# Optimization experiments

Measured on AMD Instinct MI355X. Metric: run time of the kernel, lower is better.

## Reference

```python
import jax, jax.numpy as jnp
import numpy as np
from jax import lax

N, T, D, W, H, V = 256, 64, 1280, 256, 512, 10000
NULL_IDX = 0  # ignore_index


def setup_inputs() -> dict:
    key = jax.random.key(0)
    ks = jax.random.split(key, 9)
    features = jax.random.normal(ks[0], (N, D), dtype=jnp.float32)
    captions = jax.random.randint(ks[1], (N, T + 1), 0, V, dtype=jnp.int64)
    # learned parameters
    W_proj = jax.random.normal(ks[2], (D, H), dtype=jnp.float32) / np.sqrt(D)
    b_proj = jnp.zeros((H,), dtype=jnp.float32)
    W_embed = jax.random.normal(ks[3], (V, W), dtype=jnp.float32) / np.sqrt(V)
    Wx = jax.random.normal(ks[4], (W, H), dtype=jnp.float32) / np.sqrt(W)
    Wh = jax.random.normal(ks[5], (H, H), dtype=jnp.float32) / np.sqrt(H)
    b = jnp.zeros((H,), dtype=jnp.float32)
    W_out = jax.random.normal(ks[6], (H, V), dtype=jnp.float32) / np.sqrt(H)
    b_out = jnp.zeros((V,), dtype=jnp.float32)
    return {"features": features, "captions": captions, "W_proj": W_proj,
            "b_proj": b_proj, "W_embed": W_embed, "Wx": Wx, "Wh": Wh, "b": b,
            "W_out": W_out, "b_out": b_out}


def reference(features, captions, W_proj, b_proj, W_embed, Wx, Wh, b, W_out, b_out):
    captions_in = captions[:, :-1]   # (N, T)
    captions_out = captions[:, 1:]   # (N, T)

    h0 = features @ W_proj + b_proj                      # (N, H)
    x = W_embed[captions_in]                             # (N, T, W)
    # Precompute input-to-hidden part; recurrence only needs h @ Wh.
    xWxb = jnp.einsum('ntw,wh->nth', x, Wx) + b          # (N, T, H)

    def step(h_prev, xt):
        h_next = jnp.tanh(h_prev @ Wh + xt)
        return h_next, h_next

    _, hs = lax.scan(step, h0, jnp.swapaxes(xWxb, 0, 1))  # (T, N, H)
    h = jnp.swapaxes(hs, 0, 1)                            # (N, T, H)

    scores = jnp.einsum('nth,hv->ntv', h, W_out) + b_out  # (N, T, V)
    logp = jax.nn.log_softmax(scores, axis=-1)
    nll = -jnp.take_along_axis(logp, captions_out[..., None], axis=-1)[..., 0]
    mask = (captions_out != NULL_IDX).astype(nll.dtype)
    loss = jnp.sum(nll * mask) / N
    return loss
```

## Files before the change

kernel.cpp:

```cpp
#include <hip/hip_runtime.h>
#include <hip/hip_bf16.h>
#include <hip/hip_fp8.h>

#define NB 256
#define TT 64
#define DD 1280
#define WW 256
#define HH 512
#define VV 10000
#define VP 10112
#define NCT 79
#define MROWS (NB*TT)

typedef short short8 __attribute__((ext_vector_type(8)));
typedef float f32x4 __attribute__((ext_vector_type(4)));
typedef int   int4v __attribute__((ext_vector_type(4)));
typedef int   int8v __attribute__((ext_vector_type(8)));

static __device__ __forceinline__ unsigned short f2bf(float x){
    unsigned int u = __float_as_uint(x);
    unsigned int r = u + 0x7FFFu + ((u >> 16) & 1u);
    return (unsigned short)(r >> 16);
}
static __device__ __forceinline__ float bf2f(unsigned short u){
    return __uint_as_float(((unsigned int)u) << 16);
}
static __device__ __forceinline__ unsigned char f2f8(float x){
    __hip_fp8_e4m3 q(x);
    return (unsigned char)q.__x;
}
static __device__ __forceinline__ unsigned enc4(float x){
    unsigned s = (x < 0.f) ? 8u : 0u;
    float a = fabsf(x);
    unsigned m;
    if      (a < 0.25f) m = 0;
    else if (a < 0.75f) m = 1;
    else if (a < 1.25f) m = 2;
    else if (a < 1.75f) m = 3;
    else if (a < 2.5f)  m = 4;
    else if (a < 3.5f)  m = 5;
    else if (a < 5.0f)  m = 6;
    else                m = 7;
    return s | m;
}
static __device__ __forceinline__ void gload16b(const unsigned char* g, unsigned char* l){
    __builtin_amdgcn_global_load_lds(
        (const __attribute__((address_space(1))) void*)g,
        (__attribute__((address_space(3))) void*)l, 16, 0, 0);
}


__global__ __launch_bounds__(256) void k_convbf(const float* __restrict__ in,
                                                unsigned short* __restrict__ out, int n4){
    int i = blockIdx.x*256 + threadIdx.x;
    if (i < n4){
        float4 f = *reinterpret_cast<const float4*>(in + (size_t)i*4);
        unsigned short* o = out + (size_t)i*4;
        o[0]=f2bf(f.x); o[1]=f2bf(f.y); o[2]=f2bf(f.z); o[3]=f2bf(f.w);
    }
}

__global__ __launch_bounds__(256) void k_transpose_bf(const float* __restrict__ in,
                                                      unsigned short* __restrict__ out,
                                                      int R, int C, int Cp){
    __shared__ unsigned short tile[64][17];
    int r0 = blockIdx.y*16, c0 = blockIdx.x*64;
    int tid = threadIdx.x;
    int c = tid & 63, rr = tid >> 6;
    #pragma unroll
    for (int j = 0; j < 4; ++j){
        int r = rr + j*4;
        unsigned short v = 0;
        if (r0 + r < R && c0 + c < C) v = f2bf(in[(size_t)(r0+r)*C + c0 + c]);
        tile[c][r] = v;
    }
    __syncthreads();
    int rw = tid & 15, cw = tid >> 4;
    #pragma unroll
    for (int j = 0; j < 4; ++j){
        int c2 = cw + j*16;
        if (c0 + c2 < Cp && r0 + rw < R)
            out[(size_t)(c0+c2)*R + r0 + rw] = tile[c2][rw];
    }
}

__global__ __launch_bounds__(256) void k_transpose_f8(const float* __restrict__ in,
                                                      unsigned char* __restrict__ out,
                                                      int R, int C, int Cp){
    __shared__ unsigned char tile[64][20];
    int r0 = blockIdx.y*16, c0 = blockIdx.x*64;
    int tid = threadIdx.x;
    int c = tid & 63, rr = tid >> 6;
    #pragma unroll
    for (int j = 0; j < 4; ++j){
        int r = rr + j*4;
        unsigned char v = 0;
        if (r0 + r < R && c0 + c < C) v = f2f8(in[(size_t)(r0+r)*C + c0 + c]);
        tile[c][r] = v;
    }
    __syncthreads();
    int rw = tid & 15, cw = tid >> 4;
    #pragma unroll
    for (int j = 0; j < 4; ++j){
        int c2 = cw + j*16;
        int col = c0 + c2, k = r0 + rw;
        if (col < Cp && k < R){
            size_t addr = ((size_t)((col >> 7)*4 + (k >> 7)))*16384
                        + (unsigned)((col & 127)*128 + (k & 127));
            out[addr] = tile[c2][rw];
        }
    }
}

__global__ __launch_bounds__(512) void k_wh4(const float* __restrict__ Wh,
                                             unsigned char* __restrict__ WhT4){
    int j = blockIdx.x;
    int col = threadIdx.x;
    float w0 = Wh[(size_t)(2*j  )*HH + col] * 32.0f;
    float w1 = Wh[(size_t)(2*j+1)*HH + col] * 32.0f;
    WhT4[(size_t)col*256 + j] = (unsigned char)(enc4(w0) | (enc4(w1) << 4));
}

__global__ __launch_bounds__(256) void k_biaspad(const float* __restrict__ bo, float* __restrict__ bop){
    int i = blockIdx.x*256 + threadIdx.x;
    if (i < VP) bop[i] = (i < VV) ? bo[i] : -30000.0f;
}

__global__ __launch_bounds__(512) void k_h0(const float* __restrict__ feat,
                                            const unsigned short* __restrict__ Wpb,
                                            const float* __restrict__ bp,
                                            float* __restrict__ h0){
    int n0 = blockIdx.x*2;
    int h = threadIdx.x;
    const float* f0 = feat + (size_t)(n0+0)*DD;
    const float* f1 = feat + (size_t)(n0+1)*DD;
    float a0=0.f, a1=0.f;
    for (int d = 0; d < DD; d += 4){
        #pragma unroll
        for (int j = 0; j < 4; ++j){
            float w = bf2f(Wpb[(size_t)(d+j)*HH + h]);
            a0 += f0[d+j]*w;
            a1 += f1[d+j]*w;
        }
    }
    float bb = bp[h];
    h0[(size_t)(n0+0)*HH+h] = a0+bb;
    h0[(size_t)(n0+1)*HH+h] = a1+bb;
}

__global__ __launch_bounds__(256) void k_e2(const float* __restrict__ We,
                                            const unsigned short* __restrict__ WxT,
                                            const float* __restrict__ bias,
                                            unsigned short* __restrict__ E2b){
    int lane = threadIdx.x & 63;
    int wv   = threadIdx.x >> 6;
    int l15 = lane & 15, lhi = lane >> 4;
    int rbase = blockIdx.x*64 + wv*16;
    int arow = rbase + l15; if (arow > VV-1) arow = VV-1;
    short8 a[8];
    #pragma unroll
    for (int kk = 0; kk < 8; ++kk){
        const float* src = We + (size_t)arow*WW + kk*32 + lhi*8;
        float4 g0 = *reinterpret_cast<const float4*>(src);
        float4 g1 = *reinterpret_cast<const float4*>(src + 4);
        short8 v;
        v[0]=(short)f2bf(g0.x); v[1]=(short)f2bf(g0.y); v[2]=(short)f2bf(g0.z); v[3]=(short)f2bf(g0.w);
        v[4]=(short)f2bf(g1.x); v[5]=(short)f2bf(g1.y); v[6]=(short)f2bf(g1.z); v[7]=(short)f2bf(g1.w);
        a[kk] = v;
    }
    int ct0 = blockIdx.y*16;
    for (int ct = ct0; ct < ct0+16; ++ct){
        int c0 = ct*16;
        f32x4 acc = {0.f,0.f,0.f,0.f};
        #pragma unroll
        for (int kk = 0; kk < 8; ++kk){
            short8 b = *reinterpret_cast<const short8*>(WxT + (size_t)(c0 + l15)*WW + kk*32 + lhi*8);
            acc = __builtin_amdgcn_mfma_f32_16x16x32_bf16(a[kk], b, acc, 0, 0, 0);
        }
        float bb = bias[c0 + l15];
        #pragma unroll
        for (int r = 0; r < 4; ++r){
            int row = rbase + lhi*4 + r;
            if (row < VV) E2b[(size_t)row*HH + c0 + l15] = f2bf(acc[r] + bb);
        }
    }
}

__global__ __launch_bounds__(512, 2) void k_rnn(const float* __restrict__ h0,
                                                const unsigned char* __restrict__ WhT4,
                                                const unsigned short* __restrict__ E2b,
                                                const int* __restrict__ caps,
                                                unsigned char* __restrict__ hA8){
    __shared__ __align__(32) unsigned char hl[2][HH];
    int tid = threadIdx.x;
    int lane = tid & 63, wv = tid >> 6;
    int l15 = lane & 15, lhi = lane >> 4;
    int n = blockIdx.x;
    int c0w = wv*64;
    int mycol = c0w + lane;
    unsigned char* hbase = hA8 + ((size_t)((n>>1)*4 + (wv>>1)))*16384
                               + (unsigned)((n&1)*64*128 + (mycol & 127));

    int4v b[4][4];
    #pragma unroll
    for (int ct = 0; ct < 4; ++ct){
        int col = c0w + ct*16 + l15;
        #pragma unroll
        for (int kt = 0; kt < 4; ++kt){
            b[ct][kt] = *reinterpret_cast<const int4v*>(WhT4 + (size_t)col*256 + kt*64 + lhi*16);
            asm volatile("" : "+v"(b[ct][kt]));
        }
    }
    hl[0][tid] = f2f8(h0[(size_t)n*HH + tid]);
    __syncthreads();
    int cur = 0;
    for (int t = 0; t < TT; ++t){
        int tok = caps[n*(TT+1) + t];
        unsigned short xv = E2b[(size_t)tok*HH + mycol];
        int8v a[4];
        #pragma unroll
        for (int kt = 0; kt < 4; ++kt)
            a[kt] = *reinterpret_cast<const int8v*>(&hl[cur][kt*128 + lhi*32]);
        f32x4 acc[4];
        #pragma unroll
        for (int ct = 0; ct < 4; ++ct){
            acc[ct] = (f32x4){0.f,0.f,0.f,0.f};
            #pragma unroll
            for (int kt = 0; kt < 4; ++kt){
                int8v bb = __builtin_shufflevector(b[ct][kt], b[ct][kt], 0,1,2,3,0,1,2,3);
                acc[ct] = __builtin_amdgcn_mfma_scale_f32_16x16x128_f8f6f4(
                    a[kt], bb, acc[ct],
                    0, 4,
                    0, (int)0x7F7F7F7F,
                    0, (int)0x7A7A7A7A);
            }
        }
        float v = (lhi == 0) ? acc[0][0] : (lhi == 1) ? acc[1][0]
                : (lhi == 2) ? acc[2][0] : acc[3][0];
        float x = v + bf2f(xv);
        float e = __expf(2.f*x);
        float th = 1.f - 2.f/(e + 1.f);
        unsigned char hv = f2f8(th);
        hl[cur^1][mycol] = hv;
        hbase[t*128] = hv;
        __syncthreads();
        cur ^= 1;
    }
}

__global__ __launch_bounds__(256) void k_scores(const unsigned char* __restrict__ hA8,
                                                const unsigned char* __restrict__ WoT8p,
                                                const float* __restrict__ bop,
                                                const int* __restrict__ caps,
                                                float* __restrict__ pps,
                                                float* __restrict__ pts){
    __shared__ unsigned char As[128*128];
    __shared__ unsigned char Bs[128*128];
    int bid = blockIdx.x;
    int x = bid & 7;
    int local = bid >> 3;
    int ct = local >> 4;
    int rt = x*16 + (local & 15);

    int tid = threadIdx.x;
    int lane = tid & 63, wv = tid >> 6;
    int l15 = lane & 15, lhi = lane >> 4;
    int wr = wv >> 1, wc = wv & 1;
    const unsigned char* Abase = hA8   + (size_t)rt*65536;
    const unsigned char* Bbase = WoT8p + (size_t)ct*65536;

    unsigned coff[4];
    #pragma unroll
    for (int i = 0; i < 4; ++i){
        unsigned chunk = (unsigned)(i*256 + tid);
        unsigned rowloc = chunk >> 3;
        coff[i] = rowloc*128 + (((chunk & 7u) ^ (rowloc & 7u))*16u);
    }

    f32x4 acc[4][4];
    #pragma unroll
    for (int m = 0; m < 4; ++m)
        #pragma unroll
        for (int n = 0; n < 4; ++n)
            acc[m][n] = (f32x4){0.f,0.f,0.f,0.f};

    for (int kt = 0; kt < 4; ++kt){
        #pragma unroll
        for (int i = 0; i < 4; ++i){
            gload16b(Abase + kt*16384 + coff[i], As + (unsigned)((i*256 + wv*64) * 16));
            gload16b(Bbase + kt*16384 + coff[i], Bs + (unsigned)((i*256 + wv*64) * 16));
        }
        __syncthreads();
        int8v af[4], bf[4];
        #pragma unroll
        for (int m = 0; m < 4; ++m){
            unsigned row = (unsigned)(wr*64 + m*16 + l15);
            int4v c0 = *reinterpret_cast<const int4v*>(As + row*128 + (((unsigned)(lhi*2+0) ^ (row&7))*16));
            int4v c1 = *reinterpret_cast<const int4v*>(As + row*128 + (((unsigned)(lhi*2+1) ^ (row&7))*16));
            af[m] = __builtin_shufflevector(c0, c1, 0,1,2,3,4,5,6,7);
        }
        #pragma unroll
        for (int n = 0; n < 4; ++n){
            unsigned col = (unsigned)(wc*64 + n*16 + l15);
            int4v c0 = *reinterpret_cast<const int4v*>(Bs + col*128 + (((unsigned)(lhi*2+0) ^ (col&7))*16));
            int4v c1 = *reinterpret_cast<const int4v*>(Bs + col*128 + (((unsigned)(lhi*2+1) ^ (col&7))*16));
            bf[n] = __builtin_shufflevector(c0, c1, 0,1,2,3,4,5,6,7);
        }
        #pragma unroll
        for (int m = 0; m < 4; ++m)
            #pragma unroll
            for (int n = 0; n < 4; ++n)
                acc[m][n] = __builtin_amdgcn_mfma_scale_f32_16x16x128_f8f6f4(
                    af[m], bf[n], acc[m][n],
                    0, 0,
                    0, (int)0x7F7F7F7F,
                    0, (int)0x7F7F7F7F);
        __syncthreads();
    }

    int tg[4][4];
    float srun[4][4], ts[4][4];
    #pragma unroll
    for (int m = 0; m < 4; ++m)
        #pragma unroll
        for (int r = 0; r < 4; ++r){
            int gr = rt*128 + wr*64 + m*16 + lhi*4 + r;
            tg[m][r] = caps[(gr >> 6)*(TT+1) + (gr & 63) + 1];
            srun[m][r] = 0.f; ts[m][r] = 0.f;
        }
    #pragma unroll
    for (int n = 0; n < 4; ++n){
        int colg = ct*128 + wc*64 + n*16 + l15;
        float bb = bop[colg];
        #pragma unroll
        for (int m = 0; m < 4; ++m)
            #pragma unroll
            for (int r = 0; r < 4; ++r){
                float sc = acc[m][n][r] + bb;
                srun[m][r] += __expf(sc);
                if (tg[m][r] == colg) ts[m][r] += sc;
            }
    }
    #pragma unroll
    for (int off = 1; off < 16; off <<= 1)
        #pragma unroll
        for (int m = 0; m < 4; ++m)
            #pragma unroll
            for (int r = 0; r < 4; ++r){
                srun[m][r] += __shfl_xor(srun[m][r], off, 64);
                ts[m][r]   += __shfl_xor(ts[m][r],   off, 64);
            }
    float* red = (float*)As;
    if (wc == 1 && l15 == 0){
        #pragma unroll
        for (int m = 0; m < 4; ++m)
            #pragma unroll
            for (int r = 0; r < 4; ++r){
                int ri = wr*64 + m*16 + lhi*4 + r;
                red[ri]       = srun[m][r];
                red[128 + ri] = ts[m][r];
            }
    }
    __syncthreads();
    if (wc == 0 && l15 == 0){
        #pragma unroll
        for (int m = 0; m < 4; ++m)
            #pragma unroll
            for (int r = 0; r < 4; ++r){
                int ri = wr*64 + m*16 + lhi*4 + r;
                int gr = rt*128 + ri;
                pps[(size_t)ct*MROWS + gr] = srun[m][r] + red[ri];
                pts[(size_t)ct*MROWS + gr] = ts[m][r]   + red[128 + ri];
            }
    }
}

__global__ __launch_bounds__(256) void k_loss1(const float* __restrict__ pps,
                                               const float* __restrict__ pts,
                                               const int* __restrict__ caps,
                                               float* __restrict__ bsum){
    __shared__ float reds[256], redt[256];
    int tid = threadIdx.x;
    int rloc = tid & 63, q = tid >> 6;
    int row = blockIdx.x*64 + rloc;
    int c0 = q*20, c1 = (q == 3) ? NCT : c0 + 20;
    float s = 0.f, t0 = 0.f;
    for (int ct = c0; ct < c1; ++ct){
        s  += pps[(size_t)ct*MROWS + row];
        t0 += pts[(size_t)ct*MROWS + row];
    }
    reds[tid] = s; redt[tid] = t0;
    __syncthreads();
    if (q == 0){
        s  = reds[rloc] + reds[64+rloc] + reds[128+rloc] + reds[192+rloc];
        t0 = redt[rloc] + redt[64+rloc] + redt[128+rloc] + redt[192+rloc];
        int tgt = caps[(row >> 6)*(TT+1) + (row & 63) + 1];
        reds[rloc] = (tgt != 0) ? (__logf(s) - t0) : 0.f;
    }
    __syncthreads();
    if (tid < 32) reds[tid] += reds[tid+32];
    __syncthreads();
    if (tid < 16) reds[tid] += reds[tid+16];
    __syncthreads();
    if (tid < 8)  reds[tid] += reds[tid+8];
    __syncthreads();
    if (tid < 4)  reds[tid] += reds[tid+4];
    __syncthreads();
    if (tid == 0) bsum[blockIdx.x] = reds[0] + reds[1] + reds[2] + reds[3];
}

__global__ __launch_bounds__(64) void k_loss2(const float* __restrict__ bsum, float* __restrict__ out){
    __shared__ float red[64];
    int tid = threadIdx.x;
    red[tid] = bsum[tid] + bsum[tid+64] + bsum[tid+128] + bsum[tid+192];
    __syncthreads();
    for (int off = 32; off > 0; off >>= 1){
        if (tid < off) red[tid] += red[tid+off];
        __syncthreads();
    }
    if (tid == 0) out[0] = red[0] / (float)NB;
}

extern "C" void kernel_launch(void* const* d_in, const int* in_sizes, int n_in,
                              void* d_out, int out_size, void* d_ws, size_t ws_size,
                              hipStream_t stream) {
    const float* features = (const float*)d_in[0];
    const int*   captions = (const int*)  d_in[1];
    const float* W_proj   = (const float*)d_in[2];
    const float* b_proj   = (const float*)d_in[3];
    const float* W_embed  = (const float*)d_in[4];
    const float* Wx       = (const float*)d_in[5];
    const float* Wh       = (const float*)d_in[6];
    const float* b_       = (const float*)d_in[7];
    const float* W_out    = (const float*)d_in[8];
    const float* b_out    = (const float*)d_in[9];
    float* out = (float*)d_out;

    char* ws = (char*)d_ws;
    unsigned short* E2b   = (unsigned short*)(ws + 0);
    float*          h0    = (float*)         (ws + 10240000);
    unsigned char*  WhT4  = (unsigned char*) (ws + 10764288);
    unsigned short* WxT   = (unsigned short*)(ws + 10895360);
    unsigned char*  WoT8p = (unsigned char*) (ws + 11157504);
    float*          bop   = (float*)         (ws + 16334848);
    unsigned char*  hA8   = (unsigned char*) (ws + 16375296);
    float*          pps   = (float*)         (ws + 24763904);
    float*          pts   = (float*)         (ws + 29941248);
    float*          bsum  = (float*)         (ws + 35118592);
    unsigned short* Wpb   = (unsigned short*)(ws + 35119616);
    if (ws_size < 36430336u) return;

    k_convbf<<<640, 256, 0, stream>>>(W_proj, Wpb, DD*HH/4);
    k_transpose_bf<<<dim3(8, 16),  256, 0, stream>>>(Wx,    WxT,   WW, HH, HH);
    k_wh4<<<256, 512, 0, stream>>>(Wh, WhT4);
    k_transpose_f8<<<dim3(158,32), 256, 0, stream>>>(W_out, WoT8p, HH, VV, VP);
    k_biaspad<<<40, 256, 0, stream>>>(b_out, bop);
    k_h0<<<NB/2, 512, 0, stream>>>(features, Wpb, b_proj, h0);
    k_e2<<<dim3(157,2), 256, 0, stream>>>(W_embed, WxT, b_, E2b);
    k_rnn<<<NB, 512, 0, stream>>>(h0, WhT4, E2b, captions, hA8);
    k_scores<<<128*NCT, 256, 0, stream>>>(hA8, WoT8p, bop, captions, pps, pts);
    k_loss1<<<256, 256, 0, stream>>>(pps, pts, captions, bsum);
    k_loss2<<<1, 64, 0, stream>>>(bsum, out);
}
```

Measured before the change: 339.5 us.

## Fuse weight-prep kernels into one launch and load two K-tiles per sync in scores

Five small weight-preparation kernels (bf16 convert, Wx transpose, Wh 4-bit pack, W_out fp8 transpose, bias pad) are merged into a single k_prep launch that dispatches on block index. This removes four kernel launches and the serialization gaps between them. Separately, the scores GEMM now stages two 128-wide K tiles into doubled LDS buffers per barrier pair, halving the number of syncs. The larger LDS footprint (64KB per block) may lower occupancy of the scores kernel.

```diff
diff --git a/kernel.cpp b/kernel.cpp
--- a/kernel.cpp
+++ b/kernel.cpp
@@ -50,80 +50,75 @@
 }
 
 
-__global__ __launch_bounds__(256) void k_convbf(const float* __restrict__ in,
-                                                unsigned short* __restrict__ out, int n4){
-    int i = blockIdx.x*256 + threadIdx.x;
-    if (i < n4){
-        float4 f = *reinterpret_cast<const float4*>(in + (size_t)i*4);
-        unsigned short* o = out + (size_t)i*4;
+__global__ __launch_bounds__(256) void k_prep(const float* __restrict__ W_proj,
+                                              unsigned short* __restrict__ Wpb,
+                                              const float* __restrict__ Wx,
+                                              unsigned short* __restrict__ WxT,
+                                              const float* __restrict__ Wh,
+                                              unsigned char* __restrict__ WhT4,
+                                              const float* __restrict__ W_out,
+                                              unsigned char* __restrict__ WoT8p,
+                                              const float* __restrict__ bo,
+                                              float* __restrict__ bop){
+    __shared__ unsigned short tileS[64][17];
+    int b = blockIdx.x;
+    int tid = threadIdx.x;
+    if (b < 640){
+        int i = b*256 + tid;
+        float4 f = *reinterpret_cast<const float4*>(W_proj + (size_t)i*4);
+        unsigned short* o = Wpb + (size_t)i*4;
         o[0]=f2bf(f.x); o[1]=f2bf(f.y); o[2]=f2bf(f.z); o[3]=f2bf(f.w);
-    }
-}
-
-__global__ __launch_bounds__(256) void k_transpose_bf(const float* __restrict__ in,
-                                                      unsigned short* __restrict__ out,
-                                                      int R, int C, int Cp){
-    __shared__ unsigned short tile[64][17];
-    int r0 = blockIdx.y*16, c0 = blockIdx.x*64;
-    int tid = threadIdx.x;
-    int c = tid & 63, rr = tid >> 6;
-    #pragma unroll
-    for (int j = 0; j < 4; ++j){
-        int r = rr + j*4;
-        unsigned short v = 0;
-        if (r0 + r < R && c0 + c < C) v = f2bf(in[(size_t)(r0+r)*C + c0 + c]);
-        tile[c][r] = v;
-    }
-    __syncthreads();
-    int rw = tid & 15, cw = tid >> 4;
-    #pragma unroll
-    for (int j = 0; j < 4; ++j){
-        int c2 = cw + j*16;
-        if (c0 + c2 < Cp && r0 + rw < R)
-            out[(size_t)(c0+c2)*R + r0 + rw] = tile[c2][rw];
-    }
-}
-
-__global__ __launch_bounds__(256) void k_transpose_f8(const float* __restrict__ in,
-                                                      unsigned char* __restrict__ out,
-                                                      int R, int C, int Cp){
-    __shared__ unsigned char tile[64][20];
-    int r0 = blockIdx.y*16, c0 = blockIdx.x*64;
-    int tid = threadIdx.x;
-    int c = tid & 63, rr = tid >> 6;
-    #pragma unroll
-    for (int j = 0; j < 4; ++j){
-        int r = rr + j*4;
-        unsigned char v = 0;
-        if (r0 + r < R && c0 + c < C) v = f2f8(in[(size_t)(r0+r)*C + c0 + c]);
-        tile[c][r] = v;
-    }
-    __syncthreads();
-    int rw = tid & 15, cw = tid >> 4;
-    #pragma unroll
-    for (int j = 0; j < 4; ++j){
-        int c2 = cw + j*16;
-        int col = c0 + c2, k = r0 + rw;
-        if (col < Cp && k < R){
-            size_t addr = ((size_t)((col >> 7)*4 + (k >> 7)))*16384
-                        + (unsigned)((col & 127)*128 + (k & 127));
-            out[addr] = tile[c2][rw];
-        }
-    }
-}
-
-__global__ __launch_bounds__(512) void k_wh4(const float* __restrict__ Wh,
-                                             unsigned char* __restrict__ WhT4){
-    int j = blockIdx.x;
-    int col = threadIdx.x;
-    float w0 = Wh[(size_t)(2*j  )*HH + col] * 32.0f;
-    float w1 = Wh[(size_t)(2*j+1)*HH + col] * 32.0f;
-    WhT4[(size_t)col*256 + j] = (unsigned char)(enc4(w0) | (enc4(w1) << 4));
-}
-
-__global__ __launch_bounds__(256) void k_biaspad(const float* __restrict__ bo, float* __restrict__ bop){
-    int i = blockIdx.x*256 + threadIdx.x;
-    if (i < VP) bop[i] = (i < VV) ? bo[i] : -30000.0f;
+    } else if (b < 768){
+        int r = b - 640;
+        int c0 = (r & 7)*64, r0 = (r >> 3)*16;
+        int c = tid & 63, rr = tid >> 6;
+        #pragma unroll
+        for (int j = 0; j < 4; ++j){
+            int rw_ = rr + j*4;
+            tileS[c][rw_] = f2bf(Wx[(size_t)(r0+rw_)*HH + c0 + c]);
+        }
+        __syncthreads();
+        int rw = tid & 15, cw = tid >> 4;
+        #pragma unroll
+        for (int j = 0; j < 4; ++j){
+            int c2 = cw + j*16;
+            WxT[(size_t)(c0+c2)*WW + r0 + rw] = tileS[c2][rw];
+        }
+    } else if (b < 1280){
+        int r = b - 768;
+        int j = r >> 1;
+        int col = (r & 1)*256 + tid;
+        float w0 = Wh[(size_t)(2*j  )*HH + col] * 32.0f;
+        float w1 = Wh[(size_t)(2*j+1)*HH + col] * 32.0f;
+        WhT4[(size_t)col*256 + j] = (unsigned char)(enc4(w0) | (enc4(w1) << 4));
+    } else if (b < 6336){
+        unsigned char (*tileC)[20] = reinterpret_cast<unsigned char (*)[20]>(&tileS[0][0]);
+        int r = b - 1280;
+        int c0 = (r % 158)*64, r0 = (r / 158)*16;
+        int c = tid & 63, rr = tid >> 6;
+        #pragma unroll
+        for (int j = 0; j < 4; ++j){
+            int rw_ = rr + j*4;
+            unsigned char v = 0;
+            if (c0 + c < VV) v = f2f8(W_out[(size_t)(r0+rw_)*VV + c0 + c]);
+            tileC[c][rw_] = v;
+        }
+        __syncthreads();
+        int rw = tid & 15, cw = tid >> 4;
+        #pragma unroll
+        for (int j = 0; j < 4; ++j){
+            int c2 = cw + j*16;
+            int col = c0 + c2, k = r0 + rw;
+            if (col < VP){
+                size_t addr = ((size_t)((col >> 7)*4 + (k >> 7)))*16384
+                            + (unsigned)((col & 127)*128 + (k & 127));
+                WoT8p[addr] = tileC[c2][rw];
+            }
+        }
+    } else {
+        int i = (b - 6336)*256 + tid;
+        if (i < VP) bop[i] = (i < VV) ? bo[i] : -30000.0f;
+    }
 }
 
 __global__ __launch_bounds__(512) void k_h0(const float* __restrict__ feat,
@@ -254,8 +249,8 @@
                                                 const int* __restrict__ caps,
                                                 float* __restrict__ pps,
                                                 float* __restrict__ pts){
-    __shared__ unsigned char As[128*128];
-    __shared__ unsigned char Bs[128*128];
+    __shared__ unsigned char As[2*16384];
+    __shared__ unsigned char Bs[2*16384];
     int bid = blockIdx.x;
     int x = bid & 7;
     int local = bid >> 3;
@@ -284,37 +279,46 @@
         for (int n = 0; n < 4; ++n)
             acc[m][n] = (f32x4){0.f,0.f,0.f,0.f};
 
-    for (int kt = 0; kt < 4; ++kt){
-        #pragma unroll
-        for (int i = 0; i < 4; ++i){
-            gload16b(Abase + kt*16384 + coff[i], As + (unsigned)((i*256 + wv*64) * 16));
-            gload16b(Bbase + kt*16384 + coff[i], Bs + (unsigned)((i*256 + wv*64) * 16));
-        }
-        __syncthreads();
-        int8v af[4], bf[4];
-        #pragma unroll
-        for (int m = 0; m < 4; ++m){
-            unsigned row = (unsigned)(wr*64 + m*16 + l15);
-            int4v c0 = *reinterpret_cast<const int4v*>(As + row*128 + (((unsigned)(lhi*2+0) ^ (row&7))*16));
-            int4v c1 = *reinterpret_cast<const int4v*>(As + row*128 + (((unsigned)(lhi*2+1) ^ (row&7))*16));
-            af[m] = __builtin_shufflevector(c0, c1, 0,1,2,3,4,5,6,7);
-        }
-        #pragma unroll
-        for (int n = 0; n < 4; ++n){
-            unsigned col = (unsigned)(wc*64 + n*16 + l15);
-            int4v c0 = *reinterpret_cast<const int4v*>(Bs + col*128 + (((unsigned)(lhi*2+0) ^ (col&7))*16));
-            int4v c1 = *reinterpret_cast<const int4v*>(Bs + col*128 + (((unsigned)(lhi*2+1) ^ (col&7))*16));
-            bf[n] = __builtin_shufflevector(c0, c1, 0,1,2,3,4,5,6,7);
-        }
-        #pragma unroll
-        for (int m = 0; m < 4; ++m)
-            #pragma unroll
-            for (int n = 0; n < 4; ++n)
-                acc[m][n] = __builtin_amdgcn_mfma_scale_f32_16x16x128_f8f6f4(
-                    af[m], bf[n], acc[m][n],
-                    0, 0,
-                    0, (int)0x7F7F7F7F,
-                    0, (int)0x7F7F7F7F);
+    for (int kt2 = 0; kt2 < 2; ++kt2){
+        #pragma unroll
+        for (int s = 0; s < 2; ++s){
+            int kt = kt2*2 + s;
+            #pragma unroll
+            for (int i = 0; i < 4; ++i){
+                gload16b(Abase + kt*16384 + coff[i], As + s*16384 + (unsigned)((i*256 + wv*64)*16));
+                gload16b(Bbase + kt*16384 + coff[i], Bs + s*16384 + (unsigned)((i*256 + wv*64)*16));
+            }
+        }
+        __syncthreads();
+        #pragma unroll
+        for (int s = 0; s < 2; ++s){
+            const unsigned char* Ak = As + s*16384;
+            const unsigned char* Bk = Bs + s*16384;
+            int8v af[4], bf[4];
+            #pragma unroll
+            for (int m = 0; m < 4; ++m){
+                unsigned row = (unsigned)(wr*64 + m*16 + l15);
+                int4v c0 = *reinterpret_cast<const int4v*>(Ak + row*128 + (((unsigned)(lhi*2+0) ^ (row&7))*16));
+                int4v c1 = *reinterpret_cast<const int4v*>(Ak + row*128 + (((unsigned)(lhi*2+1) ^ (row&7))*16));
+                af[m] = __builtin_shufflevector(c0, c1, 0,1,2,3,4,5,6,7);
+            }
+            #pragma unroll
+            for (int n = 0; n < 4; ++n){
+                unsigned col = (unsigned)(wc*64 + n*16 + l15);
+                int4v c0 = *reinterpret_cast<const int4v*>(Bk + col*128 + (((unsigned)(lhi*2+0) ^ (col&7))*16));
+                int4v c1 = *reinterpret_cast<const int4v*>(Bk + col*128 + (((unsigned)(lhi*2+1) ^ (col&7))*16));
+                bf[n] = __builtin_shufflevector(c0, c1, 0,1,2,3,4,5,6,7);
+            }
+            #pragma unroll
+            for (int m = 0; m < 4; ++m)
+                #pragma unroll
+                for (int n = 0; n < 4; ++n)
+                    acc[m][n] = __builtin_amdgcn_mfma_scale_f32_16x16x128_f8f6f4(
+                        af[m], bf[n], acc[m][n],
+                        0, 0,
+                        0, (int)0x7F7F7F7F,
+                        0, (int)0x7F7F7F7F);
+        }
         __syncthreads();
     }
 
@@ -450,11 +454,7 @@
     unsigned short* Wpb   = (unsigned short*)(ws + 35119616);
     if (ws_size < 36430336u) return;
 
-    k_convbf<<<640, 256, 0, stream>>>(W_proj, Wpb, DD*HH/4);
-    k_transpose_bf<<<dim3(8, 16),  256, 0, stream>>>(Wx,    WxT,   WW, HH, HH);
-    k_wh4<<<256, 512, 0, stream>>>(Wh, WhT4);
-    k_transpose_f8<<<dim3(158,32), 256, 0, stream>>>(W_out, WoT8p, HH, VV, VP);
-    k_biaspad<<<40, 256, 0, stream>>>(b_out, bop);
+    k_prep<<<6376, 256, 0, stream>>>(W_proj, Wpb, Wx, WxT, Wh, WhT4, W_out, WoT8p, b_out, bop);
     k_h0<<<NB/2, 512, 0, stream>>>(features, Wpb, b_proj, h0);
     k_e2<<<dim3(157,2), 256, 0, stream>>>(W_embed, WxT, b_, E2b);
     k_rnn<<<NB, 512, 0, stream>>>(h0, WhT4, E2b, captions, hA8);
```

New measurement: 326.2 us. 3.9% less time.
